# Performance work log

Measured on AMD Instinct MI355X. Metric: run time of the kernel, lower is better.

## Reference

```python
import jax, jax.numpy as jnp
import numpy as np

BATCH, IN_DIM, UNITS = 1048576, 128, 128


def setup_inputs() -> dict:
    key = jax.random.key(0)
    kx, ks, kv = jax.random.split(key, 3)
    x = jax.random.normal(kx, (BATCH, IN_DIM), dtype=jnp.float32)
    # s_factors ~ N(mu=1.0, sigma=0.1) in the original init
    s = 1.0 + 0.1 * jax.random.normal(ks, (IN_DIM,), dtype=jnp.float32)
    V = jax.random.normal(kv, (IN_DIM, UNITS), dtype=jnp.float32) * (1.0 / np.sqrt(IN_DIM))
    bias = jnp.zeros((UNITS,), dtype=jnp.float32)
    return {"x": x, "s": s, "V": V, "bias": bias}


def reference(x, s, V, bias):
    # W = diag(exp(s)) @ V  ==  exp(s)[:, None] * V  (row-wise scale)
    W = jnp.exp(s)[:, None] * V  # [in_dim, units]
    return jnp.tanh(x @ W + bias)  # [batch, units]
```

## Files before the change

### kernel.cpp

```cpp
#include <hip/hip_runtime.h>
#include <hip/hip_bf16.h>
#include <math.h>


typedef _Float16 half8 __attribute__((ext_vector_type(8)));
typedef float float4v __attribute__((ext_vector_type(4)));

#define RWF_BATCH   1048576
#define RWF_K       128
#define RWF_N       128
#define RWF_TILE_M  64
#define RWF_NTILES  (RWF_BATCH / RWF_TILE_M)
#define RWF_GRID    2048

__global__ void rwf_setup_w(const float* __restrict__ s,
                            const float* __restrict__ V,
                            _Float16* __restrict__ wsT) {
    int t = blockIdx.x * blockDim.x + threadIdx.x;
    int i = t >> 7;
    int j = t & 127;
    float w = expf(s[i]) * V[t];
    _Float16 hi = (_Float16)w;
    _Float16 lo = (_Float16)(w - (float)hi);
    wsT[j * 128 + i]         = hi;
    wsT[16384 + j * 128 + i] = lo;
}

__global__ __launch_bounds__(256, 2) void rwf_main(
    const float* __restrict__ x,
    const float* __restrict__ bias,
    const _Float16* __restrict__ wsT,
    float* __restrict__ out)
{
    const int lane = threadIdx.x & 63;
    const int wave = threadIdx.x >> 6;
    const int ln15 = lane & 15;
    const int quad = lane >> 4;

    const int wrow = (wave >> 1) * 32;
    const int wcol = (wave & 1) * 64;

    half8 bh[4][4], bl[4][4];
    #pragma unroll
    for (int ks = 0; ks < 4; ++ks) {
        #pragma unroll
        for (int nt = 0; nt < 4; ++nt) {
            int n   = wcol + nt * 16 + ln15;
            int off = n * 128 + ks * 32 + quad * 8;
            bh[ks][nt] = *(const half8*)(wsT + off);
            bl[ks][nt] = *(const half8*)(wsT + 16384 + off);
        }
    }

    float bv[4];
    #pragma unroll
    for (int nt = 0; nt < 4; ++nt) bv[nt] = bias[wcol + nt * 16 + ln15];

    for (int tile = blockIdx.x; tile < RWF_NTILES; tile += gridDim.x) {
        const int row0 = tile * RWF_TILE_M + wrow;

        float4v acc[2][4];
        #pragma unroll
        for (int mt = 0; mt < 2; ++mt)
            #pragma unroll
            for (int nt = 0; nt < 4; ++nt)
                acc[mt][nt] = (float4v)0.0f;

        #pragma unroll
        for (int ks = 0; ks < 4; ++ks) {
            half8 a[2];
            #pragma unroll
            for (int mt = 0; mt < 2; ++mt) {
                const float* p = x + (size_t)(row0 + mt * 16 + ln15) * RWF_K
                                   + ks * 32 + quad * 8;
                float4v u0 = *(const float4v*)p;
                float4v u1 = *(const float4v*)(p + 4);
                half8 av;
                av[0] = (_Float16)u0[0]; av[1] = (_Float16)u0[1];
                av[2] = (_Float16)u0[2]; av[3] = (_Float16)u0[3];
                av[4] = (_Float16)u1[0]; av[5] = (_Float16)u1[1];
                av[6] = (_Float16)u1[2]; av[7] = (_Float16)u1[3];
                a[mt] = av;
            }
            #pragma unroll
            for (int mt = 0; mt < 2; ++mt) {
                #pragma unroll
                for (int nt = 0; nt < 4; ++nt) {
                    acc[mt][nt] = __builtin_amdgcn_mfma_f32_16x16x32_f16(
                        a[mt], bh[ks][nt], acc[mt][nt], 0, 0, 0);
                    acc[mt][nt] = __builtin_amdgcn_mfma_f32_16x16x32_f16(
                        a[mt], bl[ks][nt], acc[mt][nt], 0, 0, 0);
                }
            }
        }

        #pragma unroll
        for (int mt = 0; mt < 2; ++mt) {
            #pragma unroll
            for (int nt = 0; nt < 4; ++nt) {
                #pragma unroll
                for (int r = 0; r < 4; ++r) {
                    int row = row0 + mt * 16 + quad * 4 + r;
                    int col = wcol + nt * 16 + ln15;
                    float z = acc[mt][nt][r] + bv[nt];
                    float e = __expf(2.0f * z);
                    float o = 1.0f - 2.0f * __builtin_amdgcn_rcpf(e + 1.0f);
                    out[(size_t)row * RWF_N + col] = o;
                }
            }
        }
    }
}

extern "C" void kernel_launch(void* const* d_in, const int* in_sizes, int n_in,
                              void* d_out, int out_size, void* d_ws, size_t ws_size,
                              hipStream_t stream) {
    const float* x    = (const float*)d_in[0];
    const float* s    = (const float*)d_in[1];
    const float* V    = (const float*)d_in[2];
    const float* bias = (const float*)d_in[3];
    float* out        = (float*)d_out;
    _Float16* wsT     = (_Float16*)d_ws;

    rwf_setup_w<<<(RWF_K * RWF_N) / 256, 256, 0, stream>>>(s, V, wsT);
    rwf_main<<<RWF_GRID, 256, 0, stream>>>(x, bias, wsT, out);
}
```

Measured before the change: 929.3 us.

## Drop fp16 split-weight correction, rewarp tile layout, fold bias, use nontemporal stores

Removes the hi/lo fp16 split of W, so each output tile needs half as many MFMAs and the weights occupy half the registers. Each wave now covers all 64 rows of a tile and a 32-column strip instead of a 32x64 quadrant, the bias is preloaded into the accumulators, and launch bounds rise to allow 4 blocks per CU. Output stores become nontemporal. The kernel is memory-bound on x and out, so the main gains would come from higher occupancy and the store hint. The cost is reduced accuracy, because W is now rounded to plain fp16, and each x row is now loaded redundantly by all four waves.

```diff
diff --git a/kernel.cpp b/kernel.cpp
--- a/kernel.cpp
+++ b/kernel.cpp
@@ -1,5 +1,4 @@
 #include <hip/hip_runtime.h>
-#include <hip/hip_bf16.h>
 #include <math.h>
 
 
@@ -20,13 +19,10 @@
     int i = t >> 7;
     int j = t & 127;
     float w = expf(s[i]) * V[t];
-    _Float16 hi = (_Float16)w;
-    _Float16 lo = (_Float16)(w - (float)hi);
-    wsT[j * 128 + i]         = hi;
-    wsT[16384 + j * 128 + i] = lo;
+    wsT[j * 128 + i] = (_Float16)w;
 }
 
-__global__ __launch_bounds__(256, 2) void rwf_main(
+__global__ __launch_bounds__(256, 4) void rwf_main(
     const float* __restrict__ x,
     const float* __restrict__ bias,
     const _Float16* __restrict__ wsT,
@@ -36,43 +32,44 @@
     const int wave = threadIdx.x >> 6;
     const int ln15 = lane & 15;
     const int quad = lane >> 4;
+    const int wcol = wave * 32;
 
-    const int wrow = (wave >> 1) * 32;
-    const int wcol = (wave & 1) * 64;
-
-    half8 bh[4][4], bl[4][4];
+    half8 bh[4][2];
     #pragma unroll
     for (int ks = 0; ks < 4; ++ks) {
         #pragma unroll
-        for (int nt = 0; nt < 4; ++nt) {
-            int n   = wcol + nt * 16 + ln15;
-            int off = n * 128 + ks * 32 + quad * 8;
-            bh[ks][nt] = *(const half8*)(wsT + off);
-            bl[ks][nt] = *(const half8*)(wsT + 16384 + off);
+        for (int nt = 0; nt < 2; ++nt) {
+            int n = wcol + nt * 16 + ln15;
+            bh[ks][nt] = *(const half8*)(wsT + n * 128 + ks * 32 + quad * 8);
         }
     }
 
-    float bv[4];
+    float bv[2];
     #pragma unroll
-    for (int nt = 0; nt < 4; ++nt) bv[nt] = bias[wcol + nt * 16 + ln15];
+    for (int nt = 0; nt < 2; ++nt) bv[nt] = bias[wcol + nt * 16 + ln15];
+
+    const int laneoff = ln15 * RWF_K + quad * 8;
 
     for (int tile = blockIdx.x; tile < RWF_NTILES; tile += gridDim.x) {
-        const int row0 = tile * RWF_TILE_M + wrow;
+        const float* xb = x + (size_t)tile * RWF_TILE_M * RWF_K;
 
-        float4v acc[2][4];
+        float4v acc[4][2];
         #pragma unroll
-        for (int mt = 0; mt < 2; ++mt)
+        for (int mt = 0; mt < 4; ++mt)
             #pragma unroll
-            for (int nt = 0; nt < 4; ++nt)
-                acc[mt][nt] = (float4v)0.0f;
+            for (int nt = 0; nt < 2; ++nt) {
+                acc[mt][nt][0] = bv[nt];
+                acc[mt][nt][1] = bv[nt];
+                acc[mt][nt][2] = bv[nt];
+                acc[mt][nt][3] = bv[nt];
+            }
 
         #pragma unroll
         for (int ks = 0; ks < 4; ++ks) {
-            half8 a[2];
+            half8 a[4];
             #pragma unroll
-            for (int mt = 0; mt < 2; ++mt) {
-                const float* p = x + (size_t)(row0 + mt * 16 + ln15) * RWF_K
-                                   + ks * 32 + quad * 8;
+            for (int mt = 0; mt < 4; ++mt) {
+                const float* p = xb + mt * 16 * RWF_K + ks * 32 + laneoff;
                 float4v u0 = *(const float4v*)p;
                 float4v u1 = *(const float4v*)(p + 4);
                 half8 av;
@@ -83,29 +80,29 @@
                 a[mt] = av;
             }
             #pragma unroll
-            for (int mt = 0; mt < 2; ++mt) {
+            for (int mt = 0; mt < 4; ++mt) {
                 #pragma unroll
-                for (int nt = 0; nt < 4; ++nt) {
+                for (int nt = 0; nt < 2; ++nt) {
                     acc[mt][nt] = __builtin_amdgcn_mfma_f32_16x16x32_f16(
                         a[mt], bh[ks][nt], acc[mt][nt], 0, 0, 0);
-                    acc[mt][nt] = __builtin_amdgcn_mfma_f32_16x16x32_f16(
-                        a[mt], bl[ks][nt], acc[mt][nt], 0, 0, 0);
                 }
             }
         }
 
+        const int row0 = tile * RWF_TILE_M + quad * 4;
+        const int col0 = wcol + ln15;
         #pragma unroll
-        for (int mt = 0; mt < 2; ++mt) {
+        for (int mt = 0; mt < 4; ++mt) {
             #pragma unroll
-            for (int nt = 0; nt < 4; ++nt) {
+            for (int nt = 0; nt < 2; ++nt) {
                 #pragma unroll
                 for (int r = 0; r < 4; ++r) {
-                    int row = row0 + mt * 16 + quad * 4 + r;
-                    int col = wcol + nt * 16 + ln15;
-                    float z = acc[mt][nt][r] + bv[nt];
+                    float z = acc[mt][nt][r];
                     float e = __expf(2.0f * z);
                     float o = 1.0f - 2.0f * __builtin_amdgcn_rcpf(e + 1.0f);
-                    out[(size_t)row * RWF_N + col] = o;
+                    __builtin_nontemporal_store(
+                        o, out + (size_t)(row0 + mt * 16 + r) * RWF_N
+                               + col0 + nt * 16);
                 }
             }
         }
```

Result: slower. 988.0 us (+6.3%).
